# Performance work log

Measured on AMD Instinct MI355X. Metric: run time of the kernel, lower is better.

The kernel has to match this reference:

```python
import jax, jax.numpy as jnp
import numpy as np

EMB = 1024
HEADS = 16
HEAD_DIM = EMB // HEADS


def setup_inputs() -> dict:
    key = jax.random.key(0)
    ks = jax.random.split(key, 9)
    s = 1.0 / np.sqrt(EMB)
    x = jax.random.normal(ks[0], (2, 2048, EMB), dtype=jnp.float32)
    Wq = jax.random.normal(ks[1], (EMB, EMB), dtype=jnp.float32) * s
    bq = jnp.zeros((EMB,), dtype=jnp.float32)
    Wk = jax.random.normal(ks[2], (EMB, EMB), dtype=jnp.float32) * s
    bk = jnp.zeros((EMB,), dtype=jnp.float32)
    Wv = jax.random.normal(ks[3], (EMB, EMB), dtype=jnp.float32) * s
    bv = jnp.zeros((EMB,), dtype=jnp.float32)
    Wo = jax.random.normal(ks[4], (EMB, EMB), dtype=jnp.float32) * s
    bo = jnp.zeros((EMB,), dtype=jnp.float32)
    return {"x": x, "Wq": Wq, "bq": bq, "Wk": Wk, "bk": bk,
            "Wv": Wv, "bv": bv, "Wo": Wo, "bo": bo}


def reference(x, Wq, bq, Wk, bk, Wv, bv, Wo, bo):
    B, S, E = x.shape
    # torch Linear: y = x @ W.T + b
    q = x @ Wq.T + bq
    k = x @ Wk.T + bk
    v = x @ Wv.T + bv
    # [B,S,E] -> [B,H,S,D]
    q = q.reshape(B, S, HEADS, HEAD_DIM).transpose(0, 2, 1, 3)
    k = k.reshape(B, S, HEADS, HEAD_DIM).transpose(0, 2, 1, 3)
    v = v.reshape(B, S, HEADS, HEAD_DIM).transpose(0, 2, 1, 3)
    energy = jnp.einsum('bhqd,bhkd->bhqk', q, k)
    scaling = jnp.float32(E) ** 0.5  # NOTE: sqrt(emb_size), not sqrt(head_dim), as in source
    att = jax.nn.softmax(energy / scaling, axis=-1)
    out = jnp.einsum('bhqk,bhkd->bhqd', att, v)
    out = out.transpose(0, 2, 1, 3).reshape(B, S, E)
    return out @ Wo.T + bo
```

## Files before the change

kernel.cpp:

```cpp
#include <hip/hip_runtime.h>
#include <stdint.h>


typedef _Float16 half8  __attribute__((ext_vector_type(8)));
typedef _Float16 half4v __attribute__((ext_vector_type(4)));
typedef _Float16 half2v __attribute__((ext_vector_type(2)));
typedef float    f32x4  __attribute__((ext_vector_type(4)));

#define GLD16(g, l) __builtin_amdgcn_global_load_lds(                         \
    (__attribute__((address_space(1))) void*)(g),                            \
    (__attribute__((address_space(3))) void*)(l), 16, 0, 0)

#define MFMA16(a, b, c) __builtin_amdgcn_mfma_f32_16x16x32_f16((a), (b), (c), 0, 0, 0)

#if __has_builtin(__builtin_amdgcn_exp2f)
#define EXP2(x) __builtin_amdgcn_exp2f(x)
#else
#define EXP2(x) exp2f(x)
#endif

static __device__ inline half2v pk_f16(float a, float b)
{
#if __has_builtin(__builtin_amdgcn_cvt_pkrtz)
    auto t = __builtin_amdgcn_cvt_pkrtz(a, b);
    return *(half2v*)&t;
#else
    half2v r = { (_Float16)a, (_Float16)b };
    return r;
#endif
}

__global__ void cvt_all(const float* __restrict__ x,  const float* __restrict__ wq,
                        const float* __restrict__ wk, const float* __restrict__ wv,
                        const float* __restrict__ wo, _Float16* __restrict__ xb,
                        _Float16* __restrict__ wqkv, _Float16* __restrict__ wob)
{
    int i = blockIdx.x * blockDim.x + threadIdx.x;
    const float* src; _Float16* dst; int off;
    if (i < 1048576)      { src = x;  dst = xb;                 off = i; }
    else if (i < 1310720) { src = wq; dst = wqkv;               off = i - 1048576; }
    else if (i < 1572864) { src = wk; dst = wqkv + 1048576;     off = i - 1310720; }
    else if (i < 1835008) { src = wv; dst = wqkv + 2097152;     off = i - 1572864; }
    else                  { src = wo; dst = wob;                off = i - 1835008; }
    float4 f = ((const float4*)src)[off];
    half4v h = { (_Float16)f.x, (_Float16)f.y, (_Float16)f.z, (_Float16)f.w };
    ((half4v*)dst)[off] = h;
}

template<int BN, int MODE>
__global__ __launch_bounds__(256, MODE == 0 ? 3 : 2)
void gemm_f16(const _Float16* __restrict__ A, const _Float16* __restrict__ W,
              const float* __restrict__ b0, const float* __restrict__ b1,
              const float* __restrict__ b2, _Float16* __restrict__ o0,
              _Float16* __restrict__ o1, _Float16* __restrict__ o2,
              float* __restrict__ outf, float qscale)
{
    constexpr int NI = BN / 32;
    __shared__ _Float16 lA[128 * 64];
    __shared__ _Float16 lB[BN * 64];
    const int m0 = blockIdx.y * 128, n0 = blockIdx.x * BN;
    const int tid = threadIdx.x, lane = tid & 63, w = tid >> 6;
    const int wr = (w >> 1) * 64, wc = (w & 1) * (BN / 2);
    const int lrow = lane & 15, lk4 = lane >> 4;
    f32x4 acc[4][NI] = {};

    for (int k0 = 0; k0 < 1024; k0 += 64) {
        __syncthreads();
#pragma unroll
        for (int c = 0; c < 4; ++c) {
            int sidx = c * 256 + tid;
            int row = sidx >> 3, sl = sidx & 7;
            int gc = k0 + ((sl ^ (row & 7)) << 3);
            GLD16(A + (size_t)(m0 + row) * 1024 + gc, lA + (size_t)(c * 256 + w * 64) * 8);
        }
#pragma unroll
        for (int c = 0; c < BN / 32; ++c) {
            int sidx = c * 256 + tid;
            int row = sidx >> 3, sl = sidx & 7;
            int gc = k0 + ((sl ^ (row & 7)) << 3);
            GLD16(W + (size_t)(n0 + row) * 1024 + gc, lB + (size_t)(c * 256 + w * 64) * 8);
        }
        __syncthreads();

#pragma unroll
        for (int kd = 0; kd < 2; ++kd) {
            half8 af[4], bf[NI];
#pragma unroll
            for (int mi = 0; mi < 4; ++mi) {
                int ra = wr + mi * 16 + lrow;
                af[mi] = *(const half8*)(lA + ra * 64 + (((kd * 4 + lk4) ^ (ra & 7)) * 8));
            }
#pragma unroll
            for (int ni = 0; ni < NI; ++ni) {
                int rb = wc + ni * 16 + lrow;
                bf[ni] = *(const half8*)(lB + rb * 64 + (((kd * 4 + lk4) ^ (rb & 7)) * 8));
            }
#pragma unroll
            for (int mi = 0; mi < 4; ++mi)
#pragma unroll
                for (int ni = 0; ni < NI; ++ni)
                    acc[mi][ni] = MFMA16(af[mi], bf[ni], acc[mi][ni]);
        }
    }

    if (MODE == 0) {
        const int which = n0 >> 10;
        const float* bp = which == 0 ? b0 : which == 1 ? b1 : b2;
        _Float16* outh  = which == 0 ? o0 : which == 1 ? o1 : o2;
        const float scale = which == 0 ? qscale : 1.f;
        const int nh = n0 & 1023;
        float bcol[NI];
#pragma unroll
        for (int ni = 0; ni < NI; ++ni) bcol[ni] = bp[nh + wc + ni * 16 + lrow];
#pragma unroll
        for (int mi = 0; mi < 4; ++mi)
#pragma unroll
            for (int ni = 0; ni < NI; ++ni)
#pragma unroll
                for (int r = 0; r < 4; ++r) {
                    int rg = m0 + wr + mi * 16 + lk4 * 4 + r;
                    int cg = nh + wc + ni * 16 + lrow;
                    float v = (acc[mi][ni][r] + bcol[ni]) * scale;
                    int b = rg >> 11, s = rg & 2047, h = cg >> 6, d = cg & 63;
                    outh[(((size_t)b * 16 + h) * 2048 + s) * 64 + d] = (_Float16)v;
                }
    } else {
        float bcol[NI];
#pragma unroll
        for (int ni = 0; ni < NI; ++ni) bcol[ni] = b0[n0 + wc + ni * 16 + lrow];
#pragma unroll
        for (int mi = 0; mi < 4; ++mi)
#pragma unroll
            for (int ni = 0; ni < NI; ++ni)
#pragma unroll
                for (int r = 0; r < 4; ++r) {
                    int rg = m0 + wr + mi * 16 + lk4 * 4 + r;
                    int cg = n0 + wc + ni * 16 + lrow;
                    outf[(size_t)rg * 1024 + cg] = acc[mi][ni][r] + bcol[ni];
                }
    }
}

__global__ __launch_bounds__(256)
void transpose_v(const _Float16* __restrict__ v, _Float16* __restrict__ vt)
{
    __shared__ _Float16 t[64][68];
    const int bh = blockIdx.y, s0 = blockIdx.x * 64;
    const _Float16* vh = v + (size_t)bh * 2048 * 64;
    _Float16* vth = vt + (size_t)bh * 64 * 2048;
    const int tid = threadIdx.x;
#pragma unroll
    for (int j = 0; j < 2; ++j) {
        int ch = j * 256 + tid, r = ch >> 3, c = (ch & 7) * 8;
        half8 d = *(const half8*)(vh + (size_t)(s0 + r) * 64 + c);
#pragma unroll
        for (int i = 0; i < 8; ++i) t[r][c + i] = d[i];
    }
    __syncthreads();
#pragma unroll
    for (int j = 0; j < 2; ++j) {
        int ch = j * 256 + tid, d = ch >> 3, sc = (ch & 7) * 8;
        half8 o;
#pragma unroll
        for (int i = 0; i < 8; ++i) o[i] = t[sc + i][d];
        *(half8*)(vth + (size_t)d * 2048 + s0 + sc) = o;
    }
}

#define KVB 64
#define NT  32
__global__ __launch_bounds__(256, 4)
void attn(const _Float16* __restrict__ q, const _Float16* __restrict__ k,
          const _Float16* __restrict__ vt, _Float16* __restrict__ ao)
{
    __shared__ _Float16 lK[2][KVB * 64];
    __shared__ _Float16 lV[2][64 * KVB];
    __shared__ _Float16 lP[4][16 * KVB];
    const int bid0 = blockIdx.x;
    const int bid = (bid0 & 7) * 128 + (bid0 >> 3);
    const int bh = bid >> 5, q0 = (bid & 31) * 64;
    const int b = bh >> 4, h = bh & 15;
    const int tid = threadIdx.x, lane = tid & 63, w = tid >> 6;
    const int lrow = lane & 15, lk4 = lane >> 4;
    const _Float16* qh = q + (size_t)bh * 2048 * 64;
    const _Float16* kh = k + (size_t)bh * 2048 * 64;
    const _Float16* vth = vt + (size_t)bh * 64 * 2048;

    half8 qf[2];
#pragma unroll
    for (int kd = 0; kd < 2; ++kd)
        qf[kd] = *(const half8*)(qh + (size_t)(q0 + w * 16 + lrow) * 64
                                    + kd * 32 + lk4 * 8);

    float l_ = 0.f;
    f32x4 o[4] = {};

    auto STAGE = [&](int t, int bs) {
        const int s0 = t * KVB;
#pragma unroll
        for (int c = 0; c < 2; ++c) {
            int sidx = c * 256 + tid;
            int row = sidx >> 3, sl = sidx & 7;
            GLD16(kh + (size_t)(s0 + row) * 64 + ((sl ^ (row & 7)) * 8),
                  lK[bs] + (size_t)(c * 256 + w * 64) * 8);
            GLD16(vth + (size_t)row * 2048 + s0 + ((sl ^ (row & 7)) * 8),
                  lV[bs] + (size_t)(c * 256 + w * 64) * 8);
        }
    };

    STAGE(0, 0);
    STAGE(1, 1);

#pragma unroll 2
    for (int t = 0; t < NT; ++t) {
        const int cur = t & 1;
        if (t < NT - 1) asm volatile("s_waitcnt vmcnt(4)" ::: "memory");
        else            asm volatile("s_waitcnt vmcnt(0)" ::: "memory");
        __builtin_amdgcn_s_barrier();
        __builtin_amdgcn_sched_barrier(0);

        f32x4 e[4] = {};
        __builtin_amdgcn_s_setprio(1);
#pragma unroll
        for (int kd = 0; kd < 2; ++kd)
#pragma unroll
            for (int mi = 0; mi < 4; ++mi) {
                int rk = mi * 16 + lrow;
                half8 kf = *(const half8*)(lK[cur] + rk * 64
                                           + (((kd * 4 + lk4) ^ (rk & 7)) * 8));
                e[mi] = MFMA16(kf, qf[kd], e[mi]);
            }
        __builtin_amdgcn_s_setprio(0);

#pragma unroll
        for (int mi = 0; mi < 4; ++mi) {
            float p0 = EXP2(e[mi][0]);
            float p1 = EXP2(e[mi][1]);
            float p2 = EXP2(e[mi][2]);
            float p3 = EXP2(e[mi][3]);
            l_ += (p0 + p1) + (p2 + p3);
            half2v lo = pk_f16(p0, p1), hi = pk_f16(p2, p3);
            half4v pb = { lo[0], lo[1], hi[0], hi[1] };
            int slot = (mi * 2 + (lk4 >> 1)) ^ (lrow & 7);
            *(half4v*)(lP[w] + lrow * 64 + slot * 8 + (lk4 & 1) * 4) = pb;
        }

        __builtin_amdgcn_s_setprio(1);
#pragma unroll
        for (int ks = 0; ks < 2; ++ks) {
            int slotp = (ks * 4 + lk4) ^ (lrow & 7);
            half8 pa = *(const half8*)(lP[w] + lrow * 64 + slotp * 8);
#pragma unroll
            for (int nd = 0; nd < 4; ++nd) {
                int drow = nd * 16 + lrow;
                int slot = (ks * 4 + lk4) ^ (drow & 7);
                half8 vf = *(const half8*)(lV[cur] + drow * 64 + slot * 8);
                o[nd] = MFMA16(pa, vf, o[nd]);
            }
        }
        __builtin_amdgcn_s_setprio(0);

        __builtin_amdgcn_s_barrier();
        if (t + 2 < NT) STAGE(t + 2, cur);
    }

    l_ += __shfl_xor(l_, 16);
    l_ += __shfl_xor(l_, 32);
    float linv[4];
#pragma unroll
    for (int r = 0; r < 4; ++r)
        linv[r] = 1.f / __shfl(l_, lk4 * 4 + r);
#pragma unroll
    for (int nd = 0; nd < 4; ++nd)
#pragma unroll
        for (int r = 0; r < 4; ++r) {
            int sg = q0 + w * 16 + lk4 * 4 + r;
            int d = nd * 16 + lrow;
            float val = o[nd][r] * linv[r];
            ao[((size_t)b * 2048 + sg) * 1024 + h * 64 + d] = (_Float16)val;
        }
}

extern "C" void kernel_launch(void* const* d_in, const int* in_sizes, int n_in,
                              void* d_out, int out_size, void* d_ws, size_t ws_size,
                              hipStream_t stream)
{
    const float* x  = (const float*)d_in[0];
    const float* Wq = (const float*)d_in[1];
    const float* bq = (const float*)d_in[2];
    const float* Wk = (const float*)d_in[3];
    const float* bk = (const float*)d_in[4];
    const float* Wv = (const float*)d_in[5];
    const float* bv = (const float*)d_in[6];
    const float* Wo = (const float*)d_in[7];
    const float* bo = (const float*)d_in[8];
    float* out = (float*)d_out;

    char* ws = (char*)d_ws;
    _Float16* xb   = (_Float16*)(ws);
    _Float16* vtb  = (_Float16*)(ws);
    _Float16* wqkv = (_Float16*)(ws + (8u  << 20));
    _Float16* wob  = (_Float16*)(ws + (14u << 20));
    _Float16* qb   = (_Float16*)(ws + (16u << 20));
    _Float16* kb   = (_Float16*)(ws + (24u << 20));
    _Float16* vb   = (_Float16*)(ws + (32u << 20));
    _Float16* aob  = vb;

    cvt_all<<<8192, 256, 0, stream>>>(x, Wq, Wk, Wv, Wo, xb, wqkv, wob);

    const float qscale = 1.4426950408889634f / 32.f;
    gemm_f16<128, 0><<<dim3(24, 32), 256, 0, stream>>>(
        xb, wqkv, bq, bk, bv, qb, kb, vb, nullptr, qscale);

    transpose_v<<<dim3(32, 32), 256, 0, stream>>>(vb, vtb);

    attn<<<1024, 256, 0, stream>>>(qb, kb, vtb, aob);

    gemm_f16<64, 1><<<dim3(16, 32), 256, 0, stream>>>(
        aob, wob, bo, nullptr, nullptr, nullptr, nullptr, nullptr, out, 1.f);
}
```

Before: 119.0 us.

## Switch attention to 32x32 MFMA with register-resident P via permlane swap

Rewrites the attention inner loop to use 32x32x16 MFMA tiles. Each wave now owns 32 query rows, so a block covers 128 queries and the grid is halved, which doubles K/V reuse per staged tile. The softmax probabilities are converted into the A-operand layout in registers with v_permlane32_swap instead of a round trip through the per-wave LDS P buffer, removing that LDS storage and its reads and writes. The cost is more accumulator registers per wave and lower occupancy (launch bounds drop from 4 to 2 blocks), with only 512 blocks to fill the GPU.

```diff
diff --git a/kernel.cpp b/kernel.cpp
--- a/kernel.cpp
+++ b/kernel.cpp
@@ -6,12 +6,14 @@
 typedef _Float16 half4v __attribute__((ext_vector_type(4)));
 typedef _Float16 half2v __attribute__((ext_vector_type(2)));
 typedef float    f32x4  __attribute__((ext_vector_type(4)));
+typedef float    f32x16 __attribute__((ext_vector_type(16)));
 
 #define GLD16(g, l) __builtin_amdgcn_global_load_lds(                         \
     (__attribute__((address_space(1))) void*)(g),                            \
     (__attribute__((address_space(3))) void*)(l), 16, 0, 0)
 
 #define MFMA16(a, b, c) __builtin_amdgcn_mfma_f32_16x16x32_f16((a), (b), (c), 0, 0, 0)
+#define MFMA32(a, b, c) __builtin_amdgcn_mfma_f32_32x32x16_f16((a), (b), (c), 0, 0, 0)
 
 #if __has_builtin(__builtin_amdgcn_exp2f)
 #define EXP2(x) __builtin_amdgcn_exp2f(x)
@@ -19,15 +21,10 @@
 #define EXP2(x) exp2f(x)
 #endif
 
-static __device__ inline half2v pk_f16(float a, float b)
-{
-#if __has_builtin(__builtin_amdgcn_cvt_pkrtz)
+static __device__ inline uint32_t pk_u32(float a, float b)
+{
     auto t = __builtin_amdgcn_cvt_pkrtz(a, b);
-    return *(half2v*)&t;
-#else
-    half2v r = { (_Float16)a, (_Float16)b };
-    return r;
-#endif
+    return __builtin_bit_cast(uint32_t, t);
 }
 
 __global__ void cvt_all(const float* __restrict__ x,  const float* __restrict__ wq,
@@ -169,31 +166,30 @@
 
 #define KVB 64
 #define NT  32
-__global__ __launch_bounds__(256, 4)
+__global__ __launch_bounds__(256, 2)
 void attn(const _Float16* __restrict__ q, const _Float16* __restrict__ k,
           const _Float16* __restrict__ vt, _Float16* __restrict__ ao)
 {
     __shared__ _Float16 lK[2][KVB * 64];
     __shared__ _Float16 lV[2][64 * KVB];
-    __shared__ _Float16 lP[4][16 * KVB];
     const int bid0 = blockIdx.x;
-    const int bid = (bid0 & 7) * 128 + (bid0 >> 3);
-    const int bh = bid >> 5, q0 = (bid & 31) * 64;
-    const int b = bh >> 4, h = bh & 15;
+    const int bid = (bid0 & 7) * 64 + (bid0 >> 3);
+    const int bh = bid >> 4, q0 = (bid & 15) * 128;
+    const int bb = bh >> 4, hh = bh & 15;
     const int tid = threadIdx.x, lane = tid & 63, w = tid >> 6;
-    const int lrow = lane & 15, lk4 = lane >> 4;
+    const int l31 = lane & 31, h = lane >> 5;
     const _Float16* qh = q + (size_t)bh * 2048 * 64;
     const _Float16* kh = k + (size_t)bh * 2048 * 64;
     const _Float16* vth = vt + (size_t)bh * 64 * 2048;
 
-    half8 qf[2];
-#pragma unroll
-    for (int kd = 0; kd < 2; ++kd)
-        qf[kd] = *(const half8*)(qh + (size_t)(q0 + w * 16 + lrow) * 64
-                                    + kd * 32 + lk4 * 8);
+    half8 qf[4];
+#pragma unroll
+    for (int kd = 0; kd < 4; ++kd)
+        qf[kd] = *(const half8*)(qh + (size_t)(q0 + w * 32 + l31) * 64
+                                    + kd * 16 + h * 8);
 
     float l_ = 0.f;
-    f32x4 o[4] = {};
+    f32x16 o0 = {}, o1 = {};
 
     auto STAGE = [&](int t, int bs) {
         const int s0 = t * KVB;
@@ -219,44 +215,51 @@
         __builtin_amdgcn_s_barrier();
         __builtin_amdgcn_sched_barrier(0);
 
-        f32x4 e[4] = {};
+        f32x16 e0 = {}, e1 = {};
         __builtin_amdgcn_s_setprio(1);
 #pragma unroll
-        for (int kd = 0; kd < 2; ++kd)
-#pragma unroll
-            for (int mi = 0; mi < 4; ++mi) {
-                int rk = mi * 16 + lrow;
-                half8 kf = *(const half8*)(lK[cur] + rk * 64
-                                           + (((kd * 4 + lk4) ^ (rk & 7)) * 8));
-                e[mi] = MFMA16(kf, qf[kd], e[mi]);
+        for (int kd = 0; kd < 4; ++kd) {
+            int r0 = l31,      s0l = (kd * 2 + h) ^ (r0 & 7);
+            int r1 = 32 + l31, s1l = (kd * 2 + h) ^ (r1 & 7);
+            half8 kf0 = *(const half8*)(lK[cur] + r0 * 64 + s0l * 8);
+            half8 kf1 = *(const half8*)(lK[cur] + r1 * 64 + s1l * 8);
+            e0 = MFMA32(kf0, qf[kd], e0);
+            e1 = MFMA32(kf1, qf[kd], e1);
+        }
+        __builtin_amdgcn_s_setprio(0);
+
+        half8 pa[4];
+#pragma unroll
+        for (int f = 0; f < 2; ++f) {
+            float p[16];
+#pragma unroll
+            for (int r = 0; r < 16; ++r) {
+                p[r] = EXP2(f == 0 ? e0[r] : e1[r]);
+                l_ += p[r];
             }
-        __builtin_amdgcn_s_setprio(0);
-
-#pragma unroll
-        for (int mi = 0; mi < 4; ++mi) {
-            float p0 = EXP2(e[mi][0]);
-            float p1 = EXP2(e[mi][1]);
-            float p2 = EXP2(e[mi][2]);
-            float p3 = EXP2(e[mi][3]);
-            l_ += (p0 + p1) + (p2 + p3);
-            half2v lo = pk_f16(p0, p1), hi = pk_f16(p2, p3);
-            half4v pb = { lo[0], lo[1], hi[0], hi[1] };
-            int slot = (mi * 2 + (lk4 >> 1)) ^ (lrow & 7);
-            *(half4v*)(lP[w] + lrow * 64 + slot * 8 + (lk4 & 1) * 4) = pb;
+#pragma unroll
+            for (int bq = 0; bq < 2; ++bq) {
+                uint32_t w0 = pk_u32(p[bq * 8 + 0], p[bq * 8 + 1]);
+                uint32_t w1 = pk_u32(p[bq * 8 + 2], p[bq * 8 + 3]);
+                uint32_t w2 = pk_u32(p[bq * 8 + 4], p[bq * 8 + 5]);
+                uint32_t w3 = pk_u32(p[bq * 8 + 6], p[bq * 8 + 7]);
+                asm volatile("v_permlane32_swap_b32 %0, %1" : "+v"(w0), "+v"(w2));
+                asm volatile("v_permlane32_swap_b32 %0, %1" : "+v"(w1), "+v"(w3));
+                union { uint32_t u[4]; half8 hv; } uu;
+                uu.u[0] = w0; uu.u[1] = w1; uu.u[2] = w2; uu.u[3] = w3;
+                pa[f * 2 + bq] = uu.hv;
+            }
         }
 
         __builtin_amdgcn_s_setprio(1);
 #pragma unroll
-        for (int ks = 0; ks < 2; ++ks) {
-            int slotp = (ks * 4 + lk4) ^ (lrow & 7);
-            half8 pa = *(const half8*)(lP[w] + lrow * 64 + slotp * 8);
-#pragma unroll
-            for (int nd = 0; nd < 4; ++nd) {
-                int drow = nd * 16 + lrow;
-                int slot = (ks * 4 + lk4) ^ (drow & 7);
-                half8 vf = *(const half8*)(lV[cur] + drow * 64 + slot * 8);
-                o[nd] = MFMA16(pa, vf, o[nd]);
-            }
+        for (int ks = 0; ks < 4; ++ks) {
+            int r0 = l31,      s0l = (ks * 2 + h) ^ (r0 & 7);
+            int r1 = 32 + l31, s1l = (ks * 2 + h) ^ (r1 & 7);
+            half8 vf0 = *(const half8*)(lV[cur] + r0 * 64 + s0l * 8);
+            half8 vf1 = *(const half8*)(lV[cur] + r1 * 64 + s1l * 8);
+            o0 = MFMA32(pa[ks], vf0, o0);
+            o1 = MFMA32(pa[ks], vf1, o1);
         }
         __builtin_amdgcn_s_setprio(0);
 
@@ -264,21 +267,16 @@
         if (t + 2 < NT) STAGE(t + 2, cur);
     }
 
-    l_ += __shfl_xor(l_, 16);
     l_ += __shfl_xor(l_, 32);
-    float linv[4];
-#pragma unroll
-    for (int r = 0; r < 4; ++r)
-        linv[r] = 1.f / __shfl(l_, lk4 * 4 + r);
-#pragma unroll
-    for (int nd = 0; nd < 4; ++nd)
-#pragma unroll
-        for (int r = 0; r < 4; ++r) {
-            int sg = q0 + w * 16 + lk4 * 4 + r;
-            int d = nd * 16 + lrow;
-            float val = o[nd][r] * linv[r];
-            ao[((size_t)b * 2048 + sg) * 1024 + h * 64 + d] = (_Float16)val;
-        }
+    const size_t obase = ((size_t)bb * 2048) * 1024 + hh * 64;
+#pragma unroll
+    for (int r = 0; r < 16; ++r) {
+        int qr = (r & 3) + 8 * (r >> 2) + 4 * h;
+        float linv = 1.f / __shfl(l_, qr);
+        int sg = q0 + w * 32 + qr;
+        ao[obase + (size_t)sg * 1024 + l31]      = (_Float16)(o0[r] * linv);
+        ao[obase + (size_t)sg * 1024 + 32 + l31] = (_Float16)(o1[r] * linv);
+    }
 }
 
 extern "C" void kernel_launch(void* const* d_in, const int* in_sizes, int n_in,
@@ -314,7 +312,7 @@
 
     transpose_v<<<dim3(32, 32), 256, 0, stream>>>(vb, vtb);
 
-    attn<<<1024, 256, 0, stream>>>(qb, kb, vtb, aob);
+    attn<<<512, 256, 0, stream>>>(qb, kb, vtb, aob);
 
     gemm_f16<64, 1><<<dim3(16, 32), 256, 0, stream>>>(
         aob, wob, bo, nullptr, nullptr, nullptr, nullptr, nullptr, out, 1.f);
```

Result: faster. 114.3 us (-3.9%).
